# Kernel tuning notes

Measured on AMD Instinct MI355X. Metric: run time of the kernel, lower is better.

The kernel has to match this reference:

```python
import jax, jax.numpy as jnp
import numpy as np

B, T, IN, H, L = 32, 512, 8, 1024, 3


def _gru_layer(x, W_ih, W_hh, b_ih, b_hh):
    # x: [B,T,D_in]; W_ih: [3H,D_in]; W_hh: [3H,H]; gate order r,z,n (PyTorch)
    Bx = x.shape[0]
    Hh = W_hh.shape[1]
    xg = jnp.einsum('btd,gd->btg', x, W_ih) + b_ih  # [B,T,3H] input-side gates, precomputed

    def step(h, xg_t):
        hg = h @ W_hh.T + b_hh
        xr, xz, xn = jnp.split(xg_t, 3, axis=-1)
        hr, hz, hn = jnp.split(hg, 3, axis=-1)
        r = jax.nn.sigmoid(xr + hr)
        z = jax.nn.sigmoid(xz + hz)
        n = jnp.tanh(xn + r * hn)
        h_new = (1.0 - z) * n + z * h
        return h_new, h_new

    h0 = jnp.zeros((Bx, Hh), x.dtype)
    _, ys = jax.lax.scan(step, h0, jnp.swapaxes(xg, 0, 1))  # [T,B,H]
    return jnp.swapaxes(ys, 0, 1)  # [B,T,H]


def setup_inputs() -> dict:
    key = jax.random.key(0)
    ks = jax.random.split(key, 32)
    k = 1.0 / np.sqrt(H)

    def u(kk, shape):
        return jax.random.uniform(kk, shape, jnp.float32, -k, k)

    inp = {'x': jax.random.normal(ks[0], (B, T, IN), jnp.float32)}
    i = 1
    for l in range(L):
        d_in = IN if l == 0 else H
        inp[f'W_ih{l}'] = u(ks[i], (3 * H, d_in)); i += 1
        inp[f'W_hh{l}'] = u(ks[i], (3 * H, H)); i += 1
        inp[f'b_ih{l}'] = u(ks[i], (3 * H,)); i += 1
        inp[f'b_hh{l}'] = u(ks[i], (3 * H,)); i += 1
    inp['fc1_w'] = u(ks[i], (512, H)); i += 1
    inp['fc1_b'] = u(ks[i], (512,)); i += 1
    inp['fc2_w'] = u(ks[i], (256, 512)); i += 1
    inp['fc2_b'] = u(ks[i], (256,)); i += 1
    inp['fc3_w'] = u(ks[i], (1, 256)); i += 1
    inp['fc3_b'] = u(ks[i], (1,)); i += 1
    return inp


def reference(x, W_ih0, W_hh0, b_ih0, b_hh0, W_ih1, W_hh1, b_ih1, b_hh1,
              W_ih2, W_hh2, b_ih2, b_hh2, fc1_w, fc1_b, fc2_w, fc2_b, fc3_w, fc3_b):
    h = x
    h = _gru_layer(h, W_ih0, W_hh0, b_ih0, b_hh0)
    h = _gru_layer(h, W_ih1, W_hh1, b_ih1, b_hh1)
    h = _gru_layer(h, W_ih2, W_hh2, b_ih2, b_hh2)
    h = jnp.mean(h, axis=1)  # temporal mean-pool -> [B,H]
    h = jax.nn.relu(h @ fc1_w.T + fc1_b)
    h = jax.nn.relu(h @ fc2_w.T + fc2_b)
    return h @ fc3_w.T + fc3_b  # [B,1]
```

## Files before the change

kernel.cpp:

```cpp
#include <hip/hip_runtime.h>
#include <cmath>

#define TT 512
#define BB 32
#define HH 1024
#define G3 3072

__device__ __forceinline__ void mv_phase(
    float (*wAll)[HH],
    float* stgL,
    float (*part)[12][32],
    const float* __restrict__ src,
    int wrow, int tid)
{
    const int wv = tid >> 6, l = tid & 63;
    const int ks = l >> 3, bg = l & 7;
    float acc[12][4];
#pragma unroll
    for (int r = 0; r < 12; r++) {
        acc[r][0] = 0.f; acc[r][1] = 0.f; acc[r][2] = 0.f; acc[r][3] = 0.f;
    }

    float4 ld[4];
#pragma unroll
    for (int i = 0; i < 4; i++)
        ld[i] = *(const float4*)&src[(size_t)(i * 8 + wv) * HH + l * 4];

#pragma unroll
    for (int c = 0; c < 4; c++) {
        __syncthreads();
#pragma unroll
        for (int i = 0; i < 4; i++) {
            int b = i * 8 + wv;
            *(float4*)&stgL[b * 256 + ((l ^ ((b >> 2) & 7)) << 2)] = ld[i];
        }
        __syncthreads();
        if (c < 3) {
#pragma unroll
            for (int i = 0; i < 4; i++)
                ld[i] = *(const float4*)&src[(size_t)(i * 8 + wv) * HH + (c + 1) * 256 + l * 4];
        }
        const int kw = c * 256 + wv * 32 + ks * 4;
        const int kb = wv * 8 + ks;
        float4 h4[4];
#pragma unroll
        for (int e = 0; e < 4; e++) {
            int b = bg * 4 + e;
            h4[e] = *(const float4*)&stgL[b * 256 + ((kb ^ ((b >> 2) & 7)) << 2)];
        }
#pragma unroll
        for (int r = 0; r < 12; r++) {
            float4 w4 = *(const float4*)&wAll[wrow + r][kw];
#pragma unroll
            for (int e = 0; e < 4; e++) {
                acc[r][e] = fmaf(w4.x, h4[e].x, acc[r][e]);
                acc[r][e] = fmaf(w4.y, h4[e].y, acc[r][e]);
                acc[r][e] = fmaf(w4.z, h4[e].z, acc[r][e]);
                acc[r][e] = fmaf(w4.w, h4[e].w, acc[r][e]);
            }
        }
    }
#pragma unroll
    for (int r = 0; r < 12; r++)
#pragma unroll
        for (int e = 0; e < 4; e++) {
            float v = acc[r][e];
            v += __shfl_xor(v, 16, 64);
            v += __shfl_xor(v, 32, 64);
            acc[r][e] = v;
        }
    if (l < 16) {
        int s = l >> 3, bgw = l & 7;
#pragma unroll
        for (int r = 0; r < 12; r++) {
            float4 o = make_float4(acc[r][0], acc[r][1], acc[r][2], acc[r][3]);
            *(float4*)&part[wv * 2 + s][r][bgw * 4] = o;
        }
    }
}

template<int IN_DIM>
__global__ __launch_bounds__(512, 2) void k_scan(
    const float* __restrict__ xsrc,
    const float* __restrict__ Wih,
    const float* __restrict__ Whh,
    const float* __restrict__ bih,
    const float* __restrict__ bhh,
    float* __restrict__ y,
    int* __restrict__ barx,
    float* __restrict__ pool)
{
    __shared__ float wAll[24][HH];
    __shared__ float stgL[32 * 256];
    __shared__ float part[16][12][32];
    __shared__ float bi[12], bh[12];
    __shared__ double pool_l[128];

    const int tid = threadIdx.x;
    const int j0 = blockIdx.x * 4;

    for (int i = tid; i < 12 * 256; i += 512) {
        int r = i >> 8, c4 = (i & 255) * 4;
        int g = r >> 2, jj = r & 3;
        *(float4*)&wAll[r][c4] =
            *(const float4*)&Whh[(size_t)(g * HH + j0 + jj) * HH + c4];
    }
    if (IN_DIM == HH) {
        for (int i = tid; i < 12 * 256; i += 512) {
            int r = i >> 8, c4 = (i & 255) * 4;
            int g = r >> 2, jj = r & 3;
            *(float4*)&wAll[12 + r][c4] =
                *(const float4*)&Wih[(size_t)(g * HH + j0 + jj) * HH + c4];
        }
    } else {
        if (tid < 96) {
            int r = tid >> 3, d = tid & 7;
            int g = r >> 2, jj = r & 3;
            wAll[12 + r][d] = Wih[(size_t)(g * HH + j0 + jj) * IN_DIM + d];
        }
    }
    if (tid < 12) {
        int g = tid >> 2, jj = tid & 3;
        bi[tid] = bih[g * HH + j0 + jj];
        bh[tid] = bhh[g * HH + j0 + jj];
    }
    if (tid < 128) pool_l[tid] = 0.0;
    __syncthreads();

    float hp_reg = 0.f;
    for (int t = 0; t < TT; t++) {
        double ig0 = 0.0, ig1 = 0.0, ig2 = 0.0;
        if (IN_DIM == HH) {
            mv_phase(wAll, stgL, part, xsrc + (size_t)t * BB * HH, 12, tid);
            __syncthreads();
            if (tid < 128) {
                int b = tid >> 2, jj = tid & 3;
                ig0 = bi[jj]; ig1 = bi[4 + jj]; ig2 = bi[8 + jj];
#pragma unroll
                for (int p = 0; p < 16; p++) {
                    ig0 += part[p][jj][b];
                    ig1 += part[p][4 + jj][b];
                    ig2 += part[p][8 + jj][b];
                }
            }
        }
        if (t > 0) {
            if (tid < 8) {
                const int target = 32 * t;
                while (__hip_atomic_load(&barx[tid * 16], __ATOMIC_RELAXED,
                                         __HIP_MEMORY_SCOPE_AGENT) < target)
                    __builtin_amdgcn_s_sleep(1);
            }
            __syncthreads();
            mv_phase(wAll, stgL, part, y + (size_t)(t - 1) * BB * HH, 0, tid);
            __syncthreads();
        }
        if (tid < 128) {
            int b = tid >> 2, jj = tid & 3, jg = j0 + jj;
            double hg0 = bh[jj], hg1 = bh[4 + jj], hg2 = bh[8 + jj];
            if (t > 0) {
#pragma unroll
                for (int p = 0; p < 16; p++) {
                    hg0 += part[p][jj][b];
                    hg1 += part[p][4 + jj][b];
                    hg2 += part[p][8 + jj][b];
                }
            }
            if (IN_DIM != HH) {
                const float* xp = xsrc + ((size_t)b * TT + t) * IN_DIM;
                float xv[8];
                *(float4*)&xv[0] = *(const float4*)&xp[0];
                *(float4*)&xv[4] = *(const float4*)&xp[4];
                float s0 = 0.f, s1 = 0.f, s2 = 0.f;
#pragma unroll
                for (int d = 0; d < 8; d++) {
                    s0 = fmaf(wAll[12 + jj][d], xv[d], s0);
                    s1 = fmaf(wAll[16 + jj][d], xv[d], s1);
                    s2 = fmaf(wAll[20 + jj][d], xv[d], s2);
                }
                ig0 = (double)bi[jj] + s0;
                ig1 = (double)bi[4 + jj] + s1;
                ig2 = (double)bi[8 + jj] + s2;
            }
            float rr = 1.f / (1.f + expf(-(float)(ig0 + hg0)));
            float zz = 1.f / (1.f + expf(-(float)(ig1 + hg1)));
            float nn = tanhf((float)(ig2 + (double)rr * hg2));
            float hnew = (1.f - zz) * nn + zz * hp_reg;
            hp_reg = hnew;
            __hip_atomic_store(&y[(size_t)t * BB * HH + b * HH + jg], hnew,
                               __ATOMIC_RELAXED, __HIP_MEMORY_SCOPE_AGENT);
            if (pool != nullptr) pool_l[tid] += (double)hnew;
        }
        if (t < TT - 1) {
            __syncthreads();
            if (tid == 0)
                __hip_atomic_fetch_add(&barx[(blockIdx.x & 7) * 16], 1,
                                       __ATOMIC_RELAXED, __HIP_MEMORY_SCOPE_AGENT);
        }
    }
    __syncthreads();
    if (pool != nullptr && tid < 128) {
        int b = tid >> 2, jj = tid & 3;
        pool[b * HH + j0 + jj] = (float)(pool_l[tid] * (1.0 / 512.0));
    }
}

__global__ __launch_bounds__(512, 2) void k_scan_x(
    const float* __restrict__ xg,
    const float* __restrict__ Whh,
    const float* __restrict__ bhh,
    float* __restrict__ y,
    int* __restrict__ flagx,
    double* __restrict__ pool,
    int t0, int t1)
{
    __shared__ float wAll[12][HH];
    __shared__ float stgL[32 * 256];
    __shared__ float part[16][12][32];
    __shared__ float bh[12];
    __shared__ double pool_l[128];

    const int tid = threadIdx.x;
    const int j0 = blockIdx.x * 4;

    for (int i = tid; i < 12 * 256; i += 512) {
        int r = i >> 8, c4 = (i & 255) * 4;
        int g = r >> 2, jj = r & 3;
        *(float4*)&wAll[r][c4] =
            *(const float4*)&Whh[(size_t)(g * HH + j0 + jj) * HH + c4];
    }
    if (tid < 12) bh[tid] = bhh[(tid >> 2) * HH + j0 + (tid & 3)];
    if (tid < 128) pool_l[tid] = 0.0;

    const int gb = tid >> 2, gjj = tid & 3;
    float hp_reg = 0.f;
    if (t0 > 0 && tid < 128)
        hp_reg = y[(size_t)(t0 - 1) * BB * HH + gb * HH + j0 + gjj];
    __syncthreads();

    for (int t = t0; t < t1; t++) {
        float xr = 0.f, xz = 0.f, xn = 0.f;
        if (tid < 128) {
            const float* xrow = xg + ((size_t)(t - t0) * BB + gb) * G3;
            xr = xrow[j0 + gjj];
            xz = xrow[HH + j0 + gjj];
            xn = xrow[2 * HH + j0 + gjj];
        }
        if (t > t0) {
            if (tid < 64) {
                const int target = t - t0;
                const int* fp = flagx + tid * 4;
                for (;;) {
                    int f0 = __hip_atomic_load(fp + 0, __ATOMIC_RELAXED,
                                               __HIP_MEMORY_SCOPE_AGENT);
                    int f1 = __hip_atomic_load(fp + 1, __ATOMIC_RELAXED,
                                               __HIP_MEMORY_SCOPE_AGENT);
                    int f2 = __hip_atomic_load(fp + 2, __ATOMIC_RELAXED,
                                               __HIP_MEMORY_SCOPE_AGENT);
                    int f3 = __hip_atomic_load(fp + 3, __ATOMIC_RELAXED,
                                               __HIP_MEMORY_SCOPE_AGENT);
                    int m01 = f0 < f1 ? f0 : f1;
                    int m23 = f2 < f3 ? f2 : f3;
                    int m = m01 < m23 ? m01 : m23;
                    if (__all(m >= target)) break;
                    __builtin_amdgcn_s_sleep(1);
                }
            }
            __syncthreads();
        }
        if (t > 0) {
            mv_phase(wAll, stgL, part, y + (size_t)(t - 1) * BB * HH, 0, tid);
            __syncthreads();
        }
        if (tid < 128) {
            double hg0 = bh[gjj], hg1 = bh[4 + gjj], hg2 = bh[8 + gjj];
            if (t > 0) {
#pragma unroll
                for (int p = 0; p < 16; p++) {
                    hg0 += part[p][gjj][gb];
                    hg1 += part[p][4 + gjj][gb];
                    hg2 += part[p][8 + gjj][gb];
                }
            }
            float rr = 1.f / (1.f + expf(-(xr + (float)hg0)));
            float zz = 1.f / (1.f + expf(-(xz + (float)hg1)));
            float nn = tanhf(xn + rr * (float)hg2);
            float hnew = (1.f - zz) * nn + zz * hp_reg;
            hp_reg = hnew;
            __hip_atomic_store(&y[(size_t)t * BB * HH + gb * HH + j0 + gjj], hnew,
                               __ATOMIC_RELAXED, __HIP_MEMORY_SCOPE_AGENT);
            if (pool != nullptr) pool_l[tid] += (double)hnew;
        }
        if (t < t1 - 1) {
            __syncthreads();
            if (tid == 0)
                __hip_atomic_store(&flagx[blockIdx.x], t - t0 + 1,
                                   __ATOMIC_RELAXED, __HIP_MEMORY_SCOPE_AGENT);
        }
    }
    __syncthreads();
    if (pool != nullptr && tid < 128)
        pool[gb * HH + j0 + gjj] += pool_l[tid];
}

__global__ __launch_bounds__(512) void k_poolfin(const double* __restrict__ pd,
                                                 float* __restrict__ pf)
{
    int i = blockIdx.x * 512 + threadIdx.x;
    if (i < BB * HH) pf[i] = (float)(pd[i] * (1.0 / 512.0));
}

__global__ __launch_bounds__(256, 2) void k_gemm_xg(const float* __restrict__ A,
                                                    const float* __restrict__ Bw,
                                                    const float* __restrict__ bias,
                                                    float* __restrict__ C)
{
    __shared__ float As[16][132];
    __shared__ float Bs[16][132];
    const int tid = threadIdx.x;
    const int tx = tid & 15, ty = tid >> 4;
    const int bm = blockIdx.x * 128, bn = blockIdx.y * 128;
    float acc[8][8];
#pragma unroll
    for (int i = 0; i < 8; i++)
#pragma unroll
        for (int j = 0; j < 8; j++) acc[i][j] = 0.f;

    const int srow = tid >> 1, sch = (tid & 1) * 8;
    for (int k0 = 0; k0 < HH; k0 += 16) {
        {
            const float* ap = &A[(size_t)(bm + srow) * HH + k0 + sch];
            float4 v0 = *(const float4*)ap;
            float4 v1 = *(const float4*)(ap + 4);
            As[sch + 0][srow] = v0.x; As[sch + 1][srow] = v0.y;
            As[sch + 2][srow] = v0.z; As[sch + 3][srow] = v0.w;
            As[sch + 4][srow] = v1.x; As[sch + 5][srow] = v1.y;
            As[sch + 6][srow] = v1.z; As[sch + 7][srow] = v1.w;
            const float* bp = &Bw[(size_t)(bn + srow) * HH + k0 + sch];
            float4 u0 = *(const float4*)bp;
            float4 u1 = *(const float4*)(bp + 4);
            Bs[sch + 0][srow] = u0.x; Bs[sch + 1][srow] = u0.y;
            Bs[sch + 2][srow] = u0.z; Bs[sch + 3][srow] = u0.w;
            Bs[sch + 4][srow] = u1.x; Bs[sch + 5][srow] = u1.y;
            Bs[sch + 6][srow] = u1.z; Bs[sch + 7][srow] = u1.w;
        }
        __syncthreads();
#pragma unroll
        for (int k = 0; k < 16; k++) {
            float a[8], b[8];
            *(float4*)&a[0] = *(const float4*)&As[k][ty * 8];
            *(float4*)&a[4] = *(const float4*)&As[k][ty * 8 + 4];
            *(float4*)&b[0] = *(const float4*)&Bs[k][tx * 8];
            *(float4*)&b[4] = *(const float4*)&Bs[k][tx * 8 + 4];
#pragma unroll
            for (int i = 0; i < 8; i++)
#pragma unroll
                for (int j = 0; j < 8; j++)
                    acc[i][j] = fmaf(a[i], b[j], acc[i][j]);
        }
        __syncthreads();
    }
#pragma unroll
    for (int i = 0; i < 8; i++) {
        float o[8];
#pragma unroll
        for (int j = 0; j < 8; j++) o[j] = acc[i][j] + bias[bn + tx * 8 + j];
        float* cp = &C[(size_t)(bm + ty * 8 + i) * G3 + bn + tx * 8];
        *(float4*)cp = *(float4*)&o[0];
        *(float4*)(cp + 4) = *(float4*)&o[4];
    }
}

__global__ __launch_bounds__(256) void k_gemm_xg0(const float* __restrict__ x,
                                                  const float* __restrict__ W,
                                                  const float* __restrict__ bias,
                                                  float* __restrict__ C,
                                                  int t0)
{
    __shared__ float As[128][8];
    __shared__ float Bs[128][8];
    const int tid = threadIdx.x;
    const int bm = blockIdx.x * 128, bn = blockIdx.y * 128;
    {
        int r = tid >> 1, hf = (tid & 1) * 4;
        int m = bm + r;
        int b = m & 31, tt = t0 + (m >> 5);
        *(float4*)&As[r][hf] = *(const float4*)&x[((size_t)b * TT + tt) * 8 + hf];
        *(float4*)&Bs[r][hf] = *(const float4*)&W[(size_t)(bn + r) * 8 + hf];
    }
    __syncthreads();
    const int tx = tid & 15, ty = tid >> 4;
    float acc[8][8];
#pragma unroll
    for (int i = 0; i < 8; i++)
#pragma unroll
        for (int j = 0; j < 8; j++) acc[i][j] = 0.f;
#pragma unroll
    for (int k = 0; k < 8; k++) {
        float a[8], b[8];
#pragma unroll
        for (int i = 0; i < 8; i++) a[i] = As[ty * 8 + i][k];
#pragma unroll
        for (int j = 0; j < 8; j++) b[j] = Bs[tx * 8 + j][k];
#pragma unroll
        for (int i = 0; i < 8; i++)
#pragma unroll
            for (int j = 0; j < 8; j++)
                acc[i][j] = fmaf(a[i], b[j], acc[i][j]);
    }
#pragma unroll
    for (int i = 0; i < 8; i++) {
        float o[8];
#pragma unroll
        for (int j = 0; j < 8; j++) o[j] = acc[i][j] + bias[bn + tx * 8 + j];
        float* cp = &C[(size_t)(bm + ty * 8 + i) * G3 + bn + tx * 8];
        *(float4*)cp = *(float4*)&o[0];
        *(float4*)(cp + 4) = *(float4*)&o[4];
    }
}

__global__ __launch_bounds__(256) void k_fc(const float* __restrict__ in,
                                            const float* __restrict__ w,
                                            const float* __restrict__ bias,
                                            float* __restrict__ out,
                                            int ind, int outd, int dorelu)
{
    int b = blockIdx.y;
    int o = blockIdx.x * 256 + threadIdx.x;
    if (o >= outd) return;
    const float* ip = in + (size_t)b * ind;
    const float* wp = w + (size_t)o * ind;
    double s = (double)bias[o];
    for (int k = 0; k < ind; k += 4) {
        float4 wv = *(const float4*)&wp[k];
        float4 iv = *(const float4*)&ip[k];
        s += (double)iv.x * wv.x + (double)iv.y * wv.y
           + (double)iv.z * wv.z + (double)iv.w * wv.w;
    }
    float v = (float)s;
    if (dorelu) v = fmaxf(v, 0.f);
    out[(size_t)b * outd + o] = v;
}

extern "C" void kernel_launch(void* const* d_in, const int* in_sizes, int n_in,
                              void* d_out, int out_size, void* d_ws, size_t ws_size,
                              hipStream_t stream)
{
    (void)in_sizes; (void)n_in; (void)out_size;
    const float* x    = (const float*)d_in[0];
    const float* Wih[3] = {(const float*)d_in[1], (const float*)d_in[5], (const float*)d_in[9]};
    const float* Whh[3] = {(const float*)d_in[2], (const float*)d_in[6], (const float*)d_in[10]};
    const float* bih[3] = {(const float*)d_in[3], (const float*)d_in[7], (const float*)d_in[11]};
    const float* bhh[3] = {(const float*)d_in[4], (const float*)d_in[8], (const float*)d_in[12]};
    const float* fc1w = (const float*)d_in[13];
    const float* fc1b = (const float*)d_in[14];
    const float* fc2w = (const float*)d_in[15];
    const float* fc2b = (const float*)d_in[16];
    const float* fc3w = (const float*)d_in[17];
    const float* fc3b = (const float*)d_in[18];

    int*    bars     = (int*)d_ws;
    int*    flags    = bars + 96 * 128;
    double* pooled_d = (double*)(flags + 96 * 256);
    float*  pooled_f = (float*)(pooled_d + BB * HH);
    float*  fc1o     = pooled_f + BB * HH;
    float*  fc2o     = fc1o + BB * 512;
    float*  y0       = fc2o + BB * 256;
    float*  y1       = y0 + (size_t)TT * BB * HH;
    float*  xg       = y1 + (size_t)TT * BB * HH;

    const size_t base = (size_t)((char*)xg - (char*)d_ws);
    if (ws_size < base) return;

    int CH = 0;
    for (int c = 512; c >= 16; c >>= 1) {
        if (base + (size_t)c * BB * G3 * 4 <= ws_size) { CH = c; break; }
    }

    hipMemsetAsync(bars, 0, (96 * 128 + 96 * 256) * sizeof(int), stream);
    hipMemsetAsync(pooled_d, 0, BB * HH * sizeof(double), stream);

    int binst = 0;
    if (CH > 0) {
        for (int t0 = 0; t0 < TT; t0 += CH) {
            k_gemm_xg0<<<dim3(CH * BB / 128, G3 / 128), 256, 0, stream>>>(
                x, Wih[0], bih[0], xg, t0);
            k_scan_x<<<256, 512, 0, stream>>>(
                xg, Whh[0], bhh[0], y0, flags + (binst++) * 256, nullptr, t0, t0 + CH);
        }
        float* ybuf[2] = {y0, y1};
        for (int l = 1; l <= 2; l++) {
            const float* src = ybuf[(l - 1) & 1];
            float* dst = ybuf[l & 1];
            double* pl = (l == 2) ? pooled_d : nullptr;
            for (int t0 = 0; t0 < TT; t0 += CH) {
                k_gemm_xg<<<dim3(CH * BB / 128, G3 / 128), 256, 0, stream>>>(
                    src + (size_t)t0 * BB * HH, Wih[l], bih[l], xg);
                k_scan_x<<<256, 512, 0, stream>>>(
                    xg, Whh[l], bhh[l], dst, flags + (binst++) * 256, pl, t0, t0 + CH);
            }
        }
        k_poolfin<<<(BB * HH + 511) / 512, 512, 0, stream>>>(pooled_d, pooled_f);
        k_fc<<<dim3(2, 32), 256, 0, stream>>>(pooled_f, fc1w, fc1b, fc1o, HH, 512, 1);
    } else {
        float* pooled_fb = pooled_f;
        k_scan<8><<<256, 512, 0, stream>>>(x, Wih[0], Whh[0], bih[0], bhh[0], y0,
                                           bars + (binst++) * 128, nullptr);
        k_scan<HH><<<256, 512, 0, stream>>>(y0, Wih[1], Whh[1], bih[1], bhh[1], y1,
                                            bars + (binst++) * 128, nullptr);
        k_scan<HH><<<256, 512, 0, stream>>>(y1, Wih[2], Whh[2], bih[2], bhh[2], y0,
                                            bars + (binst++) * 128, pooled_fb);
        k_fc<<<dim3(2, 32), 256, 0, stream>>>(pooled_fb, fc1w, fc1b, fc1o, HH, 512, 1);
    }

    k_fc<<<dim3(1, 32), 256, 0, stream>>>(fc1o, fc2w, fc2b, fc2o, 512, 256, 1);
    k_fc<<<dim3(1, 32), 256, 0, stream>>>(fc2o, fc3w, fc3b, (float*)d_out, 256, 1, 0);
}
```

Before: 18.39 ms.

## Load hidden state directly into registers in scan matvec, drop LDS staging

In the recurrent scan kernel, the per-step matvec no longer stages the previous hidden state through a shared-memory buffer. Each thread now loads its slice of h straight from global memory into registers and does the FMAs against LDS-resident weights. Partial sums are reduced across lanes with shuffles before being written to the partials array. The staging buffer is removed and launch bounds move from two blocks per CU to one, trading occupancy for register headroom. The direct global loads may hit L2 less efficiently than the cooperative staged loads did.

```diff
diff --git a/kernel.cpp b/kernel.cpp
--- a/kernel.cpp
+++ b/kernel.cpp
@@ -205,7 +205,7 @@
     }
 }
 
-__global__ __launch_bounds__(512, 2) void k_scan_x(
+__global__ __launch_bounds__(512, 1) void k_scan_x(
     const float* __restrict__ xg,
     const float* __restrict__ Whh,
     const float* __restrict__ bhh,
@@ -215,13 +215,14 @@
     int t0, int t1)
 {
     __shared__ float wAll[12][HH];
-    __shared__ float stgL[32 * 256];
     __shared__ float part[16][12][32];
     __shared__ float bh[12];
     __shared__ double pool_l[128];
 
     const int tid = threadIdx.x;
     const int j0 = blockIdx.x * 4;
+    const int wv = tid >> 6, l = tid & 63;
+    const int ks = l >> 3, bg = l & 7;
 
     for (int i = tid; i < 12 * 256; i += 512) {
         int r = i >> 8, c4 = (i & 255) * 4;
@@ -269,7 +270,52 @@
             __syncthreads();
         }
         if (t > 0) {
-            mv_phase(wAll, stgL, part, y + (size_t)(t - 1) * BB * HH, 0, tid);
+            const float* hsrc = y + (size_t)(t - 1) * BB * HH;
+            float4 hr[4][4];
+#pragma unroll
+            for (int c = 0; c < 4; c++)
+#pragma unroll
+                for (int e = 0; e < 4; e++)
+                    hr[c][e] = *(const float4*)
+                        &hsrc[(size_t)(bg * 4 + e) * HH + c * 256 + wv * 32 + ks * 4];
+
+            float acc[12][4];
+#pragma unroll
+            for (int r = 0; r < 12; r++) {
+                acc[r][0] = 0.f; acc[r][1] = 0.f; acc[r][2] = 0.f; acc[r][3] = 0.f;
+            }
+#pragma unroll
+            for (int c = 0; c < 4; c++) {
+                const int kw = c * 256 + wv * 32 + ks * 4;
+#pragma unroll
+                for (int r = 0; r < 12; r++) {
+                    float4 w4 = *(const float4*)&wAll[r][kw];
+#pragma unroll
+                    for (int e = 0; e < 4; e++) {
+                        acc[r][e] = fmaf(w4.x, hr[c][e].x, acc[r][e]);
+                        acc[r][e] = fmaf(w4.y, hr[c][e].y, acc[r][e]);
+                        acc[r][e] = fmaf(w4.z, hr[c][e].z, acc[r][e]);
+                        acc[r][e] = fmaf(w4.w, hr[c][e].w, acc[r][e]);
+                    }
+                }
+            }
+#pragma unroll
+            for (int r = 0; r < 12; r++)
+#pragma unroll
+                for (int e = 0; e < 4; e++) {
+                    float v = acc[r][e];
+                    v += __shfl_xor(v, 16, 64);
+                    v += __shfl_xor(v, 32, 64);
+                    acc[r][e] = v;
+                }
+            if (l < 16) {
+                int s = l >> 3, bgw = l & 7;
+#pragma unroll
+                for (int r = 0; r < 12; r++) {
+                    float4 o = make_float4(acc[r][0], acc[r][1], acc[r][2], acc[r][3]);
+                    *(float4*)&part[wv * 2 + s][r][bgw * 4] = o;
+                }
+            }
             __syncthreads();
         }
         if (tid < 128) {
```

Result: faster. 16.33 ms, median of 2 (-11.2%).
